# Performance work log

Measured on AMD Instinct MI355X. Metric: run time of the kernel, lower is better.

The kernel has to match this reference:

```python
import jax, jax.numpy as jnp
import numpy as np

B, T, U, C, V = 4, 400, 100, 512, 512

def setup_inputs() -> dict:
    key = jax.random.key(0)
    k1, k2, k3, k4 = jax.random.split(key, 4)
    encoder_out = jax.random.normal(k1, (B, T, C), dtype=jnp.float32)
    predictor_out = jax.random.normal(k2, (B, U, C), dtype=jnp.float32)
    # torch.nn.Linear default init: U(-1/sqrt(in), 1/sqrt(in))
    bound = 1.0 / np.sqrt(C)
    W = jax.random.uniform(k3, (V, C), minval=-bound, maxval=bound, dtype=jnp.float32)
    b = jax.random.uniform(k4, (V,), minval=-bound, maxval=bound, dtype=jnp.float32)
    return {"encoder_out": encoder_out, "predictor_out": predictor_out, "W": W, "b": b}

def reference(encoder_out, predictor_out, W, b):
    # broadcast add: (b,t,1,c) + (b,1,u,c) -> (b,t,u,c)
    logit = jnp.tanh(encoder_out[:, :, None, :] + predictor_out[:, None, :, :])
    # linear projection over last dim: (b,t,u,c) @ (c,v) + (v,)
    return jnp.einsum('btuc,vc->btuv', logit, W) + b
```

## Files before the change

kernel.cpp:

```cpp
#include <hip/hip_runtime.h>
#include <hip/hip_bf16.h>

typedef __attribute__((ext_vector_type(4))) float          f32x4;
typedef __attribute__((ext_vector_type(4))) int            i32x4;
typedef __attribute__((ext_vector_type(2))) unsigned int   u32x2;
typedef __attribute__((ext_vector_type(4))) unsigned int   u32x4;
typedef __attribute__((ext_vector_type(8))) unsigned short u16x8;

#define Cc 512
#define Vv 512
#define BM 64
#define NTILE 2500

#define BOUND 0.04419417382415922f
#define INV_SW (127.0f / BOUND)
#define OSCALE (BOUND / 16129.0f)

__device__ unsigned g_W2i[Vv * Cc / 4];
__device__ unsigned short g_ta[1600 * Cc];
__device__ unsigned short g_tp[400 * Cc];

__device__ __forceinline__ float fast_tanh(float x) {
    float e = __expf(2.0f * x);
    return 1.0f - 2.0f * __builtin_amdgcn_rcpf(e + 1.0f);
}

__device__ __forceinline__ unsigned cvt_pk_bf16(float lo, float hi) {
    unsigned r;
    asm("v_cvt_pk_bf16_f32 %0, %1, %2" : "=v"(r) : "v"(lo), "v"(hi));
    return r;
}

__device__ __forceinline__ float bf2f(unsigned short b) {
    return __uint_as_float(((unsigned)b) << 16);
}

__device__ __forceinline__ unsigned pack4(int q0, int q1, int q2, int q3) {
    return (q0 & 0xff) | ((q1 & 0xff) << 8) | ((q2 & 0xff) << 16) | (q3 << 24);
}

__global__ __launch_bounds__(256) void prep_kernel(
    const float* __restrict__ W, const float* __restrict__ enc,
    const float* __restrict__ pred)
{
    const int b = blockIdx.x;
    if (b < 64) {
        int gid = b * 256 + threadIdx.x;
        int v  = gid >> 5;
        int k0 = (gid & 31) * 16;
        const float* wp = W + v * Cc + k0;
        f32x4 wv[4];
#pragma unroll
        for (int c = 0; c < 4; ++c) wv[c] = *(const f32x4*)(wp + c * 4);
        u32x4 o;
#pragma unroll
        for (int c = 0; c < 4; ++c)
            o[c] = pack4(__float2int_rn(wv[c][0] * INV_SW),
                         __float2int_rn(wv[c][1] * INV_SW),
                         __float2int_rn(wv[c][2] * INV_SW),
                         __float2int_rn(wv[c][3] * INV_SW));
        int f  = (v >> 4) * 8 + (k0 >> 6);
        int ln = (v & 15) + 16 * ((k0 >> 4) & 3);
        *(u32x4*)((char*)g_W2i + f * 1024 + ln * 16) = o;
    } else if (b < 464) {
        int gid = (b - 64) * 256 + threadIdx.x;
        f32x4 a = *(const f32x4*)(enc + gid * 8);
        f32x4 c = *(const f32x4*)(enc + gid * 8 + 4);
        u32x4 o;
        o[0] = cvt_pk_bf16(fast_tanh(a[0]), fast_tanh(a[1]));
        o[1] = cvt_pk_bf16(fast_tanh(a[2]), fast_tanh(a[3]));
        o[2] = cvt_pk_bf16(fast_tanh(c[0]), fast_tanh(c[1]));
        o[3] = cvt_pk_bf16(fast_tanh(c[2]), fast_tanh(c[3]));
        *(u32x4*)(g_ta + gid * 8) = o;
    } else {
        int gid = (b - 464) * 256 + threadIdx.x;
        f32x4 a = *(const f32x4*)(pred + gid * 8);
        f32x4 c = *(const f32x4*)(pred + gid * 8 + 4);
        u32x4 o;
        o[0] = cvt_pk_bf16(fast_tanh(a[0]), fast_tanh(a[1]));
        o[1] = cvt_pk_bf16(fast_tanh(a[2]), fast_tanh(a[3]));
        o[2] = cvt_pk_bf16(fast_tanh(c[0]), fast_tanh(c[1]));
        o[3] = cvt_pk_bf16(fast_tanh(c[2]), fast_tanh(c[3]));
        *(u32x4*)(g_tp + gid * 8) = o;
    }
}

__global__ __launch_bounds__(512, 4) void joiner_main(
    const float* __restrict__ bias,
    float* __restrict__ out)
{
    __shared__ unsigned char As[BM * Cc];

    const int tid = threadIdx.x;

    const int xcd  = blockIdx.x & 7;
    const int idx  = blockIdx.x >> 3;
    const int tile = (xcd < 4 ? xcd * 313 : 4 * 313 + (xcd - 4) * 312) + idx;

    {
        const int r = tid >> 3;
        const int q = tid & 7;
        const int m  = tile * BM + r;
        const int et = m / 100;
        const int u  = m - et * 100;
        const int bb = m / 40000;
        const int pr = bb * 100 + u;
        const unsigned short* taP = g_ta + et * Cc;
        const unsigned short* tpP = g_tp + pr * Cc;
        char* asB = (char*)As;
        const int swz = (r & 7) << 4;
#pragma unroll
        for (int c = 0; c < 8; ++c) {
            const int k0 = q * 8 + c * 64;
            u16x8 ta8 = *(const u16x8*)(taP + k0);
            u16x8 tp8 = *(const u16x8*)(tpP + k0);
            int qq[8];
#pragma unroll
            for (int j = 0; j < 8; ++j) {
                float a = bf2f(ta8[j]);
                float p = bf2f(tp8[j]);
                float n = (a + p) *
                          __builtin_amdgcn_rcpf(__builtin_fmaf(a, p, 1.0f));
                qq[j] = __float2int_rn(n * 127.0f);
            }
            u32x2 o;
            o[0] = pack4(qq[0], qq[1], qq[2], qq[3]);
            o[1] = pack4(qq[4], qq[5], qq[6], qq[7]);
            int byte = r * 512 + k0;
            *(u32x2*)(asB + (byte ^ swz)) = o;
        }
    }

    const int lane = tid & 63;
    const int w    = tid >> 6;
    const int lc   = lane & 15;
    const int lkB  = (lane >> 4) << 4;

    const char* wb = (const char*)g_W2i + (size_t)(w * 4) * 8 * 1024 + lane * 16;

    i32x4 bcur[4], bnx[4];
#pragma unroll
    for (int j = 0; j < 4; ++j)
        bcur[j] = *(const i32x4*)(wb + ((j * 8 + 0) << 10));

    __syncthreads();

    i32x4 acc[4][4];
#pragma unroll
    for (int i = 0; i < 4; ++i)
#pragma unroll
        for (int j = 0; j < 4; ++j)
            acc[i][j] = (i32x4){0, 0, 0, 0};

    const char* asB = (const char*)As;
    const int aswz = (lc & 7) << 4;

#pragma unroll 2
    for (int ks = 0; ks < 8; ++ks) {
        if (ks < 7) {
#pragma unroll
            for (int j = 0; j < 4; ++j)
                bnx[j] = *(const i32x4*)(wb + ((j * 8 + ks + 1) << 10));
        }
        i32x4 af[4];
#pragma unroll
        for (int i = 0; i < 4; ++i) {
            int byte = (i * 16 + lc) * 512 + ks * 64 + lkB;
            af[i] = *(const i32x4*)(asB + (byte ^ aswz));
        }
#pragma unroll
        for (int i = 0; i < 4; ++i)
#pragma unroll
            for (int j = 0; j < 4; ++j)
                acc[i][j] = __builtin_amdgcn_mfma_i32_16x16x64_i8(
                    af[i], bcur[j], acc[i][j], 0, 0, 0);
#pragma unroll
        for (int j = 0; j < 4; ++j) bcur[j] = bnx[j];
    }

    const int lr = (lane >> 4) << 2;
    float bia[4];
#pragma unroll
    for (int j = 0; j < 4; ++j) bia[j] = bias[w * 64 + j * 16 + lc];
#pragma unroll
    for (int i = 0; i < 4; ++i) {
#pragma unroll
        for (int q = 0; q < 4; ++q) {
            size_t row = (size_t)(tile * BM + i * 16 + lr + q);
            float* op = out + row * Vv + w * 64;
#pragma unroll
            for (int j = 0; j < 4; ++j)
                __builtin_nontemporal_store(
                    __builtin_fmaf((float)acc[i][j][q], OSCALE, bia[j]),
                    op + j * 16 + lc);
        }
    }
}

extern "C" void kernel_launch(void* const* d_in, const int* in_sizes, int n_in,
                              void* d_out, int out_size, void* d_ws, size_t ws_size,
                              hipStream_t stream) {
    const float* enc  = (const float*)d_in[0];
    const float* pred = (const float*)d_in[1];
    const float* W    = (const float*)d_in[2];
    const float* bias = (const float*)d_in[3];
    float* out        = (float*)d_out;

    prep_kernel<<<564, 256, 0, stream>>>(W, enc, pred);
    joiner_main<<<NTILE, 512, 0, stream>>>(bias, out);
}
```

Baseline: 92.13 us.

## Split first 256 tiles into half-tiles to balance the tail wave

The first 256 of the 2500 row tiles are split into two 32-row half-blocks, which launches 2756 blocks instead of 2500. The aim is to ease the wave-quantization tail: with 256 CUs at up to 4 blocks each, 2500 full tiles leave an uneven last wave. Half-tile blocks run guarded MFMA, load and store loops with NI=2, and fill A with a different thread mapping. The cost is extra per-block overhead and uniform branches inside the inner loop.

```diff
diff --git a/kernel.cpp b/kernel.cpp
--- a/kernel.cpp
+++ b/kernel.cpp
@@ -10,7 +10,6 @@
 #define Cc 512
 #define Vv 512
 #define BM 64
-#define NTILE 2500
 
 #define BOUND 0.04419417382415922f
 #define INV_SW (127.0f / BOUND)
@@ -92,12 +91,21 @@
     __shared__ unsigned char As[BM * Cc];
 
     const int tid = threadIdx.x;
-
-    const int xcd  = blockIdx.x & 7;
-    const int idx  = blockIdx.x >> 3;
-    const int tile = (xcd < 4 ? xcd * 313 : 4 * 313 + (xcd - 4) * 312) + idx;
-
-    {
+    const int bid = blockIdx.x;
+
+    int tile, r0, NI;
+    if (bid < 256) {
+        tile = (bid & 7) * 32 + (bid >> 3);  r0 = 0;  NI = 2;
+    } else if (bid < 2500) {
+        int x = bid - 256, c = x & 7, i2 = x >> 3;
+        tile = 256 + (c < 4 ? c * 281 : 1124 + (c - 4) * 280) + i2;
+        r0 = 0;  NI = 4;
+    } else {
+        int x = bid - 2500;
+        tile = (x & 7) * 32 + (x >> 3);  r0 = 32;  NI = 2;
+    }
+
+    if (NI == 4) {
         const int r = tid >> 3;
         const int q = tid & 7;
         const int m  = tile * BM + r;
@@ -129,6 +137,38 @@
             int byte = r * 512 + k0;
             *(u32x2*)(asB + (byte ^ swz)) = o;
         }
+    } else {
+        const int r = tid >> 4;
+        const int q = tid & 15;
+        const int m  = tile * BM + r0 + r;
+        const int et = m / 100;
+        const int u  = m - et * 100;
+        const int bb = m / 40000;
+        const int pr = bb * 100 + u;
+        const unsigned short* taP = g_ta + et * Cc;
+        const unsigned short* tpP = g_tp + pr * Cc;
+        char* asB = (char*)As;
+        const int swz = (r & 7) << 4;
+#pragma unroll
+        for (int c = 0; c < 4; ++c) {
+            const int k0 = q * 8 + c * 128;
+            u16x8 ta8 = *(const u16x8*)(taP + k0);
+            u16x8 tp8 = *(const u16x8*)(tpP + k0);
+            int qq[8];
+#pragma unroll
+            for (int j = 0; j < 8; ++j) {
+                float a = bf2f(ta8[j]);
+                float p = bf2f(tp8[j]);
+                float n = (a + p) *
+                          __builtin_amdgcn_rcpf(__builtin_fmaf(a, p, 1.0f));
+                qq[j] = __float2int_rn(n * 127.0f);
+            }
+            u32x2 o;
+            o[0] = pack4(qq[0], qq[1], qq[2], qq[3]);
+            o[1] = pack4(qq[4], qq[5], qq[6], qq[7]);
+            int byte = r * 512 + k0;
+            *(u32x2*)(asB + (byte ^ swz)) = o;
+        }
     }
 
     const int lane = tid & 63;
@@ -165,15 +205,20 @@
         i32x4 af[4];
 #pragma unroll
         for (int i = 0; i < 4; ++i) {
-            int byte = (i * 16 + lc) * 512 + ks * 64 + lkB;
-            af[i] = *(const i32x4*)(asB + (byte ^ aswz));
-        }
-#pragma unroll
-        for (int i = 0; i < 4; ++i)
-#pragma unroll
-            for (int j = 0; j < 4; ++j)
-                acc[i][j] = __builtin_amdgcn_mfma_i32_16x16x64_i8(
-                    af[i], bcur[j], acc[i][j], 0, 0, 0);
+            if (i < NI) {
+                int byte = (i * 16 + lc) * 512 + ks * 64 + lkB;
+                af[i] = *(const i32x4*)(asB + (byte ^ aswz));
+            }
+        }
+#pragma unroll
+        for (int i = 0; i < 4; ++i) {
+            if (i < NI) {
+#pragma unroll
+                for (int j = 0; j < 4; ++j)
+                    acc[i][j] = __builtin_amdgcn_mfma_i32_16x16x64_i8(
+                        af[i], bcur[j], acc[i][j], 0, 0, 0);
+            }
+        }
 #pragma unroll
         for (int j = 0; j < 4; ++j) bcur[j] = bnx[j];
     }
@@ -184,15 +229,17 @@
     for (int j = 0; j < 4; ++j) bia[j] = bias[w * 64 + j * 16 + lc];
 #pragma unroll
     for (int i = 0; i < 4; ++i) {
-#pragma unroll
-        for (int q = 0; q < 4; ++q) {
-            size_t row = (size_t)(tile * BM + i * 16 + lr + q);
-            float* op = out + row * Vv + w * 64;
-#pragma unroll
-            for (int j = 0; j < 4; ++j)
-                __builtin_nontemporal_store(
-                    __builtin_fmaf((float)acc[i][j][q], OSCALE, bia[j]),
-                    op + j * 16 + lc);
+        if (i < NI) {
+#pragma unroll
+            for (int q = 0; q < 4; ++q) {
+                size_t row = (size_t)(tile * BM + r0 + i * 16 + lr + q);
+                float* op = out + row * Vv + w * 64;
+#pragma unroll
+                for (int j = 0; j < 4; ++j)
+                    __builtin_nontemporal_store(
+                        __builtin_fmaf((float)acc[i][j][q], OSCALE, bia[j]),
+                        op + j * 16 + lc);
+            }
         }
     }
 }
@@ -207,5 +254,5 @@
     float* out        = (float*)d_out;
 
     prep_kernel<<<564, 256, 0, stream>>>(W, enc, pred);
-    joiner_main<<<NTILE, 512, 0, stream>>>(bias, out);
-}
+    joiner_main<<<2756, 512, 0, stream>>>(bias, out);
+}
```

Measured after the change: 95.30 us. +3.4%, slower.

## Double row tile to 128 and split waves into 2x4 grid with N sub-tiles

Applied to the files above, without the earlier changes.

Raises rows per block from 64 to 128, halving the block count and the number of times each block re-reads the full quantized weight matrix. Waves become a 2x4 grid (row half by column quarter), and each wave loops over four 32-column sub-tiles with a smaller accumulator, storing each sub-tile's outputs before moving on. This interleaves stores with compute and cuts accumulator registers. The cost is a 64 KB LDS tile, which lowers how many blocks fit per CU, and more serialized per-wave work.

```diff
diff --git a/kernel.cpp b/kernel.cpp
--- a/kernel.cpp
+++ b/kernel.cpp
@@ -9,8 +9,8 @@
 
 #define Cc 512
 #define Vv 512
-#define BM 64
-#define NTILE 2500
+#define BM 128
+#define NTILE 1250
 
 #define BOUND 0.04419417382415922f
 #define INV_SW (127.0f / BOUND)
@@ -95,11 +95,11 @@
 
     const int xcd  = blockIdx.x & 7;
     const int idx  = blockIdx.x >> 3;
-    const int tile = (xcd < 4 ? xcd * 313 : 4 * 313 + (xcd - 4) * 312) + idx;
+    const int tile = (xcd < 2 ? xcd * 157 : 2 * 157 + (xcd - 2) * 156) + idx;
 
     {
-        const int r = tid >> 3;
-        const int q = tid & 7;
+        const int r = tid >> 2;
+        const int q = tid & 3;
         const int m  = tile * BM + r;
         const int et = m / 100;
         const int u  = m - et * 100;
@@ -110,8 +110,8 @@
         char* asB = (char*)As;
         const int swz = (r & 7) << 4;
 #pragma unroll
-        for (int c = 0; c < 8; ++c) {
-            const int k0 = q * 8 + c * 64;
+        for (int c = 0; c < 16; ++c) {
+            const int k0 = q * 8 + c * 32;
             u16x8 ta8 = *(const u16x8*)(taP + k0);
             u16x8 tp8 = *(const u16x8*)(tpP + k0);
             int qq[8];
@@ -133,66 +133,75 @@
 
     const int lane = tid & 63;
     const int w    = tid >> 6;
+    const int wm   = w >> 2;
+    const int wn   = w & 3;
     const int lc   = lane & 15;
     const int lkB  = (lane >> 4) << 4;
-
-    const char* wb = (const char*)g_W2i + (size_t)(w * 4) * 8 * 1024 + lane * 16;
-
-    i32x4 bcur[4], bnx[4];
-#pragma unroll
-    for (int j = 0; j < 4; ++j)
-        bcur[j] = *(const i32x4*)(wb + ((j * 8 + 0) << 10));
-
-    __syncthreads();
-
-    i32x4 acc[4][4];
-#pragma unroll
-    for (int i = 0; i < 4; ++i)
-#pragma unroll
-        for (int j = 0; j < 4; ++j)
-            acc[i][j] = (i32x4){0, 0, 0, 0};
-
+    const int lr   = (lane >> 4) << 2;
+
+    const char* wb = (const char*)g_W2i + (size_t)wn * 65536 + lane * 16;
     const char* asB = (const char*)As;
     const int aswz = (lc & 7) << 4;
+    const int rowB = (wm * 64 + lc) * 512;
+
+    i32x4 bcur[2], bnx[2];
+#pragma unroll
+    for (int jj = 0; jj < 2; ++jj)
+        bcur[jj] = *(const i32x4*)(wb + ((jj * 8 + 0) << 10));
+
+    __syncthreads();
+
+#pragma unroll
+    for (int qt = 0; qt < 4; ++qt) {
+        i32x4 acc[4][2];
+#pragma unroll
+        for (int i = 0; i < 4; ++i) { acc[i][0] = (i32x4){0,0,0,0}; acc[i][1] = (i32x4){0,0,0,0}; }
 
 #pragma unroll 2
-    for (int ks = 0; ks < 8; ++ks) {
-        if (ks < 7) {
-#pragma unroll
-            for (int j = 0; j < 4; ++j)
-                bnx[j] = *(const i32x4*)(wb + ((j * 8 + ks + 1) << 10));
-        }
-        i32x4 af[4];
-#pragma unroll
-        for (int i = 0; i < 4; ++i) {
-            int byte = (i * 16 + lc) * 512 + ks * 64 + lkB;
-            af[i] = *(const i32x4*)(asB + (byte ^ aswz));
-        }
-#pragma unroll
-        for (int i = 0; i < 4; ++i)
-#pragma unroll
-            for (int j = 0; j < 4; ++j)
-                acc[i][j] = __builtin_amdgcn_mfma_i32_16x16x64_i8(
-                    af[i], bcur[j], acc[i][j], 0, 0, 0);
-#pragma unroll
-        for (int j = 0; j < 4; ++j) bcur[j] = bnx[j];
-    }
-
-    const int lr = (lane >> 4) << 2;
-    float bia[4];
-#pragma unroll
-    for (int j = 0; j < 4; ++j) bia[j] = bias[w * 64 + j * 16 + lc];
-#pragma unroll
-    for (int i = 0; i < 4; ++i) {
-#pragma unroll
-        for (int q = 0; q < 4; ++q) {
-            size_t row = (size_t)(tile * BM + i * 16 + lr + q);
-            float* op = out + row * Vv + w * 64;
-#pragma unroll
-            for (int j = 0; j < 4; ++j)
-                __builtin_nontemporal_store(
-                    __builtin_fmaf((float)acc[i][j][q], OSCALE, bia[j]),
-                    op + j * 16 + lc);
+        for (int ks = 0; ks < 8; ++ks) {
+            if (ks < 7) {
+#pragma unroll
+                for (int jj = 0; jj < 2; ++jj)
+                    bnx[jj] = *(const i32x4*)(wb + (((qt * 2 + jj) * 8 + ks + 1) << 10));
+            }
+            i32x4 af[4];
+#pragma unroll
+            for (int i = 0; i < 4; ++i) {
+                int byte = rowB + i * 16 * 512 + ks * 64 + lkB;
+                af[i] = *(const i32x4*)(asB + (byte ^ aswz));
+            }
+#pragma unroll
+            for (int i = 0; i < 4; ++i)
+#pragma unroll
+                for (int jj = 0; jj < 2; ++jj)
+                    acc[i][jj] = __builtin_amdgcn_mfma_i32_16x16x64_i8(
+                        af[i], bcur[jj], acc[i][jj], 0, 0, 0);
+#pragma unroll
+            for (int jj = 0; jj < 2; ++jj) bcur[jj] = bnx[jj];
+        }
+
+        if (qt < 3) {
+#pragma unroll
+            for (int jj = 0; jj < 2; ++jj)
+                bcur[jj] = *(const i32x4*)(wb + ((((qt + 1) * 2 + jj) * 8 + 0) << 10));
+        }
+
+        {
+            const int cb = wn * 128 + qt * 32;
+            float b0 = bias[cb + lc];
+            float b1 = bias[cb + 16 + lc];
+#pragma unroll
+            for (int i = 0; i < 4; ++i) {
+#pragma unroll
+                for (int q4 = 0; q4 < 4; ++q4) {
+                    size_t row = (size_t)(tile * BM + wm * 64 + i * 16 + lr + q4);
+                    float* op = out + row * Vv + cb;
+                    __builtin_nontemporal_store(
+                        __builtin_fmaf((float)acc[i][0][q4], OSCALE, b0), op + lc);
+                    __builtin_nontemporal_store(
+                        __builtin_fmaf((float)acc[i][1][q4], OSCALE, b1), op + 16 + lc);
+                }
+            }
         }
     }
 }
```

Measured after the change: 93.82 us. No clear change (+1.8%).

## Switch int8 GEMM to 32x32x32 MFMA with two column passes per wave

Applied to the files above, without the earlier changes.

Replaces the 16x16x64 int8 MFMA tiling with 32x32x32 int8 MFMA. The W int8 layout is repacked to match the new fragment shape, and the LDS swizzle is widened to 16 rows. Each wave now computes its 64 output columns in two sequential 32-column passes with two accumulators, storing results after each pass. This cuts accumulator register pressure and may let the epilogue stores overlap with the second pass. In exchange it re-reads A from LDS for each pass and has less MFMA independence per iteration.

```diff
diff --git a/kernel.cpp b/kernel.cpp
--- a/kernel.cpp
+++ b/kernel.cpp
@@ -1,11 +1,12 @@
 #include <hip/hip_runtime.h>
 #include <hip/hip_bf16.h>
 
-typedef __attribute__((ext_vector_type(4))) float          f32x4;
-typedef __attribute__((ext_vector_type(4))) int            i32x4;
-typedef __attribute__((ext_vector_type(2))) unsigned int   u32x2;
-typedef __attribute__((ext_vector_type(4))) unsigned int   u32x4;
-typedef __attribute__((ext_vector_type(8))) unsigned short u16x8;
+typedef __attribute__((ext_vector_type(4)))  float          f32x4;
+typedef __attribute__((ext_vector_type(4)))  int            i32x4;
+typedef __attribute__((ext_vector_type(16))) int            i32x16;
+typedef __attribute__((ext_vector_type(2)))  unsigned int   u32x2;
+typedef __attribute__((ext_vector_type(4)))  unsigned int   u32x4;
+typedef __attribute__((ext_vector_type(8)))  unsigned short u16x8;
 
 #define Cc 512
 #define Vv 512
@@ -59,8 +60,8 @@
                          __float2int_rn(wv[c][1] * INV_SW),
                          __float2int_rn(wv[c][2] * INV_SW),
                          __float2int_rn(wv[c][3] * INV_SW));
-        int f  = (v >> 4) * 8 + (k0 >> 6);
-        int ln = (v & 15) + 16 * ((k0 >> 4) & 3);
+        int f  = (v >> 5) * 16 + (k0 >> 5);
+        int ln = (v & 31) + 32 * ((k0 >> 4) & 1);
         *(u32x4*)((char*)g_W2i + f * 1024 + ln * 16) = o;
     } else if (b < 464) {
         int gid = (b - 64) * 256 + threadIdx.x;
@@ -108,7 +109,7 @@
         const unsigned short* taP = g_ta + et * Cc;
         const unsigned short* tpP = g_tp + pr * Cc;
         char* asB = (char*)As;
-        const int swz = (r & 7) << 4;
+        const int swz = (r & 15) << 4;
 #pragma unroll
         for (int c = 0; c < 8; ++c) {
             const int k0 = q * 8 + c * 64;
@@ -133,66 +134,57 @@
 
     const int lane = tid & 63;
     const int w    = tid >> 6;
-    const int lc   = lane & 15;
-    const int lkB  = (lane >> 4) << 4;
-
-    const char* wb = (const char*)g_W2i + (size_t)(w * 4) * 8 * 1024 + lane * 16;
-
-    i32x4 bcur[4], bnx[4];
-#pragma unroll
-    for (int j = 0; j < 4; ++j)
-        bcur[j] = *(const i32x4*)(wb + ((j * 8 + 0) << 10));
+    const int lrow = lane & 31;
+    const int lkh  = lane >> 5;
+
+    const char* wb = (const char*)g_W2i + (size_t)(w * 2) * 16 * 1024 + lane * 16;
+    const char* asB = (const char*)As;
+
+    i32x4 bcur, bnx;
+    bcur = *(const i32x4*)(wb + 0);
 
     __syncthreads();
 
-    i32x4 acc[4][4];
-#pragma unroll
-    for (int i = 0; i < 4; ++i)
-#pragma unroll
-        for (int j = 0; j < 4; ++j)
-            acc[i][j] = (i32x4){0, 0, 0, 0};
-
-    const char* asB = (const char*)As;
-    const int aswz = (lc & 7) << 4;
-
-#pragma unroll 2
-    for (int ks = 0; ks < 8; ++ks) {
-        if (ks < 7) {
-#pragma unroll
-            for (int j = 0; j < 4; ++j)
-                bnx[j] = *(const i32x4*)(wb + ((j * 8 + ks + 1) << 10));
+    const int rowA0 = lrow;
+    const int rowA1 = 32 + lrow;
+    const int abyte0 = rowA0 * 512 + lkh * 16;
+    const int abyte1 = rowA1 * 512 + lkh * 16;
+    const int aswz0 = (rowA0 & 15) << 4;
+    const int aswz1 = (rowA1 & 15) << 4;
+
+    const int colBase = w * 64 + lrow;
+
+#pragma unroll
+    for (int jj = 0; jj < 2; ++jj) {
+        i32x16 acc0 = (i32x16)(0), acc1 = (i32x16)(0);
+
+#pragma unroll 4
+        for (int ks2 = 0; ks2 < 16; ++ks2) {
+            if (ks2 < 15)
+                bnx = *(const i32x4*)(wb + ((jj * 16 + ks2 + 1) << 10));
+            i32x4 a0 = *(const i32x4*)(asB + ((abyte0 + ks2 * 32) ^ aswz0));
+            i32x4 a1 = *(const i32x4*)(asB + ((abyte1 + ks2 * 32) ^ aswz1));
+            acc0 = __builtin_amdgcn_mfma_i32_32x32x32_i8(a0, bcur, acc0, 0, 0, 0);
+            acc1 = __builtin_amdgcn_mfma_i32_32x32x32_i8(a1, bcur, acc1, 0, 0, 0);
+            bcur = bnx;
         }
-        i32x4 af[4];
-#pragma unroll
-        for (int i = 0; i < 4; ++i) {
-            int byte = (i * 16 + lc) * 512 + ks * 64 + lkB;
-            af[i] = *(const i32x4*)(asB + (byte ^ aswz));
-        }
-#pragma unroll
-        for (int i = 0; i < 4; ++i)
-#pragma unroll
-            for (int j = 0; j < 4; ++j)
-                acc[i][j] = __builtin_amdgcn_mfma_i32_16x16x64_i8(
-                    af[i], bcur[j], acc[i][j], 0, 0, 0);
-#pragma unroll
-        for (int j = 0; j < 4; ++j) bcur[j] = bnx[j];
-    }
-
-    const int lr = (lane >> 4) << 2;
-    float bia[4];
-#pragma unroll
-    for (int j = 0; j < 4; ++j) bia[j] = bias[w * 64 + j * 16 + lc];
-#pragma unroll
-    for (int i = 0; i < 4; ++i) {
-#pragma unroll
-        for (int q = 0; q < 4; ++q) {
-            size_t row = (size_t)(tile * BM + i * 16 + lr + q);
-            float* op = out + row * Vv + w * 64;
-#pragma unroll
-            for (int j = 0; j < 4; ++j)
+
+        if (jj == 0)
+            bcur = *(const i32x4*)(wb + ((16 + 0) << 10));
+
+        {
+            const float bia = bias[colBase + jj * 32];
+            float* opb = out + (size_t)tile * BM * Vv + w * 64 + jj * 32 + lrow;
+#pragma unroll
+            for (int q4 = 0; q4 < 16; ++q4) {
+                int r0 = (q4 & 3) + 8 * (q4 >> 2) + 4 * lkh;
                 __builtin_nontemporal_store(
-                    __builtin_fmaf((float)acc[i][j][q], OSCALE, bia[j]),
-                    op + j * 16 + lc);
+                    __builtin_fmaf((float)acc0[q4], OSCALE, bia),
+                    opb + (size_t)r0 * Vv);
+                __builtin_nontemporal_store(
+                    __builtin_fmaf((float)acc1[q4], OSCALE, bia),
+                    opb + (size_t)(32 + r0) * Vv);
+            }
         }
     }
 }
```

Result: faster. 90.08 us (-2.2%).
